# Optimization experiments

Measured on AMD Instinct MI355X. Metric: run time of the kernel, lower is better.

The kernel has to match this reference:

```python
import jax, jax.numpy as jnp
import numpy as np

SPARSITY = 0.8
NEG_INF = -1e10


def setup_inputs() -> dict:
    key = jax.random.key(0)
    k1, k2 = jax.random.split(key)
    B, N, C = 8, 2048, 768
    x = jax.random.normal(k1, (B, N, C), dtype=jnp.float32)
    # torch nn.Linear weight layout: [out_features, in_features] = [3C, C]
    Wqkv = jax.random.normal(k2, (3 * C, C), dtype=jnp.float32) * (1.0 / np.sqrt(C))
    return {"x": x, "Wqkv": Wqkv}


def reference(x, Wqkv):
    B, N, C = x.shape
    qkv = jnp.einsum('bnc,dc->bnd', x, Wqkv)  # [B, N, 3C]
    Q, K, V = jnp.split(qkv, 3, axis=-1)
    attn = jnp.einsum('bnc,bmc->bnm', Q, K) / jnp.sqrt(jnp.float32(C))  # [B,N,N]
    k = int(N * SPARSITY)
    _, idx = jax.lax.top_k(attn, k)  # [B, N, k]
    b_ix = jnp.arange(B)[:, None, None]
    n_ix = jnp.arange(N)[None, :, None]
    mask = jnp.zeros((B, N, N), dtype=bool).at[b_ix, n_ix, idx].set(True)
    attn = jnp.where(mask, attn, jnp.float32(NEG_INF))
    attn = jax.nn.softmax(attn, axis=-1)
    return jnp.einsum('bnm,bmc->bnc', attn, V)
```

## Files before the change

### kernel.cpp

```cpp
#include <hip/hip_runtime.h>
#include <hip/hip_bf16.h>
#include <math.h>


#define BM 128
#define BN 128
#define BK 64

typedef __attribute__((ext_vector_type(8))) short bf16x8;
typedef __attribute__((ext_vector_type(4))) float f32x4;

__device__ __forceinline__ unsigned short f2bf(float f) {
    unsigned u = __float_as_uint(f);
    unsigned r = u + 0x7FFFu + ((u >> 16) & 1u);
    return (unsigned short)(r >> 16);
}
__device__ __forceinline__ float bf2f(unsigned short h) {
    return __uint_as_float(((unsigned)h) << 16);
}

__device__ __forceinline__ void async16(const void* g, void* l) {
    __builtin_amdgcn_global_load_lds(
        (const __attribute__((address_space(1))) void*)g,
        (__attribute__((address_space(3))) void*)l, 16, 0, 0);
}

struct GemmArgs {
    const unsigned short* A0;
    const unsigned short* B0;
    int lda, ldb;
    long batchA, batchB;
    float alpha;
};

template <int EPI, int NT>
__global__ __launch_bounds__(256) void gemm_bf16(
    GemmArgs g, void* Cp0, void* Cp1, int ldc, long batchC)
{
    __shared__ unsigned short As[2][BM * BK];
    __shared__ unsigned short Bs[2][BN * BK];

    const int nx  = gridDim.x, ny = gridDim.y;
    const int nwg = nx * ny * gridDim.z;
    const int flat = blockIdx.x + nx * (blockIdx.y + ny * blockIdx.z);
    const int lid  = (flat & 7) * (nwg >> 3) + (flat >> 3);
    const int bx   = lid % nx;
    const int byz  = lid / nx;
    const int by   = byz % ny;
    const int bz   = byz / ny;

    const int t    = threadIdx.x;
    const int wid  = t >> 6, lane = t & 63;
    const int wr   = wid >> 1, wc = wid & 1;
    const int fr   = lane & 15, fq = lane >> 4;
    const int m0   = by * BM, n0 = bx * BN;

    const unsigned short* Ab0 = g.A0 + (long)bz * g.batchA + (long)m0 * g.lda;
    const unsigned short* Bb0 = g.B0 + (long)bz * g.batchB + (long)n0 * g.ldb;

    const int srow = t >> 3;
    const int sgc  = ((t & 7) ^ (srow & 7)) * 8;
    const char* pa[4];
    const char* pb[4];
#pragma unroll
    for (int i = 0; i < 4; ++i) {
        pa[i] = (const char*)(Ab0 + (long)(i * 32 + srow) * g.lda + sgc);
        pb[i] = (const char*)(Bb0 + (long)(i * 32 + srow) * g.ldb + sgc);
    }

    int aoffs[4][2], boffs[4][2];
#pragma unroll
    for (int m = 0; m < 4; ++m) {
        const int ra = wr * 64 + m * 16 + fr;
        const int rb = wc * 64 + m * 16 + fr;
#pragma unroll
        for (int ks = 0; ks < 2; ++ks) {
            aoffs[m][ks] = ra * 128 + (((ks * 4 + fq) ^ (ra & 7)) * 16);
            boffs[m][ks] = rb * 128 + (((ks * 4 + fq) ^ (rb & 7)) * 16);
        }
    }
    const char* AsBase = (const char*)&As[0][0];
    const char* BsBase = (const char*)&Bs[0][0];

    f32x4 acc[4][4];
#pragma unroll
    for (int m = 0; m < 4; ++m)
#pragma unroll
        for (int n = 0; n < 4; ++n) acc[m][n] = (f32x4)0.f;

    const int ldsT = wid * 1024;

#define STAGE(kt, u)                                                          \
    {                                                                         \
        _Pragma("unroll")                                                     \
        for (int i = 0; i < 4; ++i) {                                         \
            async16(pa[i] + (kt) * 128,                                       \
                    (char*)&As[(u)][0] + i * 4096 + ldsT);                    \
            async16(pb[i] + (kt) * 128,                                       \
                    (char*)&Bs[(u)][0] + i * 4096 + ldsT);                    \
        }                                                                     \
    }

    STAGE(0, 0);

#pragma unroll
    for (int tt = 0; tt < NT; ++tt) {
        if (tt + 1 < NT) {
            STAGE(tt + 1, (tt + 1) & 1);
            asm volatile("s_waitcnt vmcnt(8)" ::: "memory");
        } else {
            asm volatile("s_waitcnt vmcnt(0)" ::: "memory");
        }
        __builtin_amdgcn_sched_barrier(0);
        __builtin_amdgcn_s_barrier();
        __builtin_amdgcn_sched_barrier(0);

        const int bufo = (tt & 1) * 16384;
        bf16x8 fA[4][2], fB[4][2];
#pragma unroll
        for (int m = 0; m < 4; ++m)
#pragma unroll
            for (int ks = 0; ks < 2; ++ks) {
                fA[m][ks] = *(const bf16x8*)(AsBase + bufo + aoffs[m][ks]);
                fB[m][ks] = *(const bf16x8*)(BsBase + bufo + boffs[m][ks]);
            }
        __builtin_amdgcn_s_setprio(1);
#pragma unroll
        for (int m = 0; m < 4; ++m)
#pragma unroll
            for (int n = 0; n < 4; ++n)
#pragma unroll
                for (int ks = 0; ks < 2; ++ks)
                    acc[m][n] = __builtin_amdgcn_mfma_f32_16x16x32_bf16(
                        fA[m][ks], fB[n][ks], acc[m][n], 0, 0, 0);
        __builtin_amdgcn_s_setprio(0);
        __builtin_amdgcn_sched_barrier(0);
        __builtin_amdgcn_s_barrier();
        __builtin_amdgcn_sched_barrier(0);
    }
#undef STAGE

#pragma unroll
    for (int m = 0; m < 4; ++m) {
        const int gr0 = m0 + wr * 64 + m * 16 + fq * 4;
#pragma unroll
        for (int n = 0; n < 4; ++n) {
            const int gc = n0 + wc * 64 + n * 16 + fr;
            if (EPI == 0) {
                float* Cf = (float*)Cp0 + (long)bz * batchC;
#pragma unroll
                for (int j = 0; j < 4; ++j)
                    Cf[(long)(gr0 + j) * ldc + gc] = g.alpha * acc[m][n][j];
            } else if (EPI == 4) {
                unsigned short* H = (unsigned short*)Cp0 + (long)bz * batchC;
#pragma unroll
                for (int j = 0; j < 4; ++j)
                    H[(long)(gr0 + j) * ldc + gc] = f2bf(g.alpha * acc[m][n][j]);
            } else {
                if (n0 < 1536) {
                    unsigned short* H = (unsigned short*)Cp0;
#pragma unroll
                    for (int j = 0; j < 4; ++j)
                        H[(long)(gr0 + j) * ldc + gc] = f2bf(acc[m][n][j]);
                } else {
                    unsigned short* Vt = (unsigned short*)Cp1;
                    ushort4 p;
                    p.x = f2bf(acc[m][n][0]); p.y = f2bf(acc[m][n][1]);
                    p.z = f2bf(acc[m][n][2]); p.w = f2bf(acc[m][n][3]);
                    const long idx =
                        ((long)(gr0 >> 11) * 768 + (gc - 1536)) * 2048 + (gr0 & 2047);
                    *(ushort4*)&Vt[idx] = p;
                }
            }
        }
    }
}

__global__ __launch_bounds__(256) void cast_bf16(
    const float* __restrict__ in, unsigned short* __restrict__ outp, int n8)
{
    const int i = blockIdx.x * 256 + threadIdx.x;
    if (i >= n8) return;
    const float4 a = ((const float4*)in)[i * 2];
    const float4 b = ((const float4*)in)[i * 2 + 1];
    ushort4 h0, h1;
    h0.x = f2bf(a.x); h0.y = f2bf(a.y); h0.z = f2bf(a.z); h0.w = f2bf(a.w);
    h1.x = f2bf(b.x); h1.y = f2bf(b.y); h1.z = f2bf(b.z); h1.w = f2bf(b.w);
    ((ushort4*)outp)[i * 2]     = h0;
    ((ushort4*)outp)[i * 2 + 1] = h1;
}

#define ROWN 2048

__global__ __launch_bounds__(256) void topk_softmax_rows(
    const unsigned short* __restrict__ Sb, unsigned short* __restrict__ P,
    int kkeep)
{
    __shared__ __align__(16) unsigned hist[2048];
    __shared__ float    redmax[4], redmin[4], ssum[4];
    __shared__ unsigned wsum[4];
    __shared__ unsigned selBin;

    const unsigned short* row = Sb + (long)blockIdx.x * ROWN;
    unsigned short* prow = P + (long)blockIdx.x * ROWN;
    const int t    = threadIdx.x;
    const int lane = t & 63, w = t >> 6;

    float x[8];
    {
        const ushort4 a = ((const ushort4*)row)[t * 2];
        const ushort4 b = ((const ushort4*)row)[t * 2 + 1];
        x[0] = bf2f(a.x); x[1] = bf2f(a.y); x[2] = bf2f(a.z); x[3] = bf2f(a.w);
        x[4] = bf2f(b.x); x[5] = bf2f(b.y); x[6] = bf2f(b.z); x[7] = bf2f(b.w);
    }
    ((uint4*)hist)[t * 2]     = make_uint4(0, 0, 0, 0);
    ((uint4*)hist)[t * 2 + 1] = make_uint4(0, 0, 0, 0);

    float mx = x[0], mn = x[0];
#pragma unroll
    for (int j = 1; j < 8; ++j) { mx = fmaxf(mx, x[j]); mn = fminf(mn, x[j]); }
#pragma unroll
    for (int off = 32; off >= 1; off >>= 1) {
        mx = fmaxf(mx, __shfl_xor(mx, off, 64));
        mn = fminf(mn, __shfl_xor(mn, off, 64));
    }
    if (lane == 0) { redmax[w] = mx; redmin[w] = mn; }
    __syncthreads();
    mx = fmaxf(fmaxf(redmax[0], redmax[1]), fmaxf(redmax[2], redmax[3]));
    mn = fminf(fminf(redmin[0], redmin[1]), fminf(redmin[2], redmin[3]));

    const float scale = 2047.0f / fmaxf(mx - mn, 1e-30f);
    int q[8];
#pragma unroll
    for (int j = 0; j < 8; ++j) {
        int v = (int)((x[j] - mn) * scale);
        q[j] = v < 0 ? 0 : (v > 2047 ? 2047 : v);
        atomicAdd(&hist[q[j]], 1u);
    }
    __syncthreads();

    const uint4 h0 = ((const uint4*)hist)[t * 2];
    const uint4 h1 = ((const uint4*)hist)[t * 2 + 1];
    const unsigned hv[8] = { h0.x, h0.y, h0.z, h0.w, h1.x, h1.y, h1.z, h1.w };
    unsigned loc = 0;
#pragma unroll
    for (int j = 0; j < 8; ++j) loc += hv[j];
    unsigned s = loc;
#pragma unroll
    for (int off = 1; off <= 32; off <<= 1) {
        const unsigned o = __shfl_down(s, off, 64);
        s += (lane + off < 64) ? o : 0u;
    }
    if (lane == 0) wsum[w] = s;
    const unsigned texcl = s - loc;
    __syncthreads();
    unsigned above = texcl;
#pragma unroll
    for (int w2 = 0; w2 < 4; ++w2)
        if (w2 > w) above += wsum[w2];
    {
        unsigned cum = above;
        int hit = -1;
#pragma unroll
        for (int j = 7; j >= 0; --j) {
            const unsigned sp = cum;
            cum += hv[j];
            if (cum >= (unsigned)kkeep && sp < (unsigned)kkeep) hit = 8 * t + j;
        }
        if (hit >= 0) selBin = (unsigned)hit;
    }
    __syncthreads();
    const int bstar = (int)selBin;

    float e[8];
    float sum = 0.f;
#pragma unroll
    for (int j = 0; j < 8; ++j) {
        e[j] = (q[j] >= bstar) ? __expf(x[j] - mx) : 0.f;
        sum += e[j];
    }
#pragma unroll
    for (int off = 32; off >= 1; off >>= 1)
        sum += __shfl_xor(sum, off, 64);
    if (lane == 0) ssum[w] = sum;
    __syncthreads();
    const float inv = 1.0f / (ssum[0] + ssum[1] + ssum[2] + ssum[3]);

    ushort4 o0, o1;
    o0.x = f2bf(e[0] * inv); o0.y = f2bf(e[1] * inv);
    o0.z = f2bf(e[2] * inv); o0.w = f2bf(e[3] * inv);
    o1.x = f2bf(e[4] * inv); o1.y = f2bf(e[5] * inv);
    o1.z = f2bf(e[6] * inv); o1.w = f2bf(e[7] * inv);
    ((ushort4*)prow)[t * 2]     = o0;
    ((ushort4*)prow)[t * 2 + 1] = o1;
}

extern "C" void kernel_launch(void* const* d_in, const int* in_sizes, int n_in,
                              void* d_out, int out_size, void* d_ws, size_t ws_size,
                              hipStream_t stream)
{
    const float* x = (const float*)d_in[0];
    const float* W = (const float*)d_in[1];
    float* out = (float*)d_out;

    const int B = 8, N = 2048, C = 768;
    const int M = B * N;
    const int kkeep = 1638;

    char* ws = (char*)d_ws;
    unsigned short* QKb = (unsigned short*)(ws);
    unsigned short* Vt  = (unsigned short*)(ws + 50331648);
    unsigned short* Sb  = (unsigned short*)(ws + 75497472);
    unsigned short* Pb  = (unsigned short*)(ws + 142606336);
    unsigned short* xb  = (unsigned short*)(ws + 75497472);
    unsigned short* Wb  = (unsigned short*)(ws + 100663296);

    cast_bf16<<<dim3(M * C / 8 / 256), 256, 0, stream>>>(x, xb, M * C / 8);
    cast_bf16<<<dim3(3 * C * C / 8 / 256), 256, 0, stream>>>(W, Wb, 3 * C * C / 8);

    {
        GemmArgs pa{};
        pa.A0 = xb; pa.B0 = Wb;
        pa.lda = C; pa.ldb = C; pa.batchA = 0; pa.batchB = 0;
        pa.alpha = 1.f;
        gemm_bf16<5, 12><<<dim3(2304 / BN, M / BM, 1), 256, 0, stream>>>(
            pa, QKb, Vt, 1536, 0);
    }
    {
        GemmArgs qk{};
        qk.A0 = QKb; qk.B0 = QKb + C;
        qk.lda = 1536; qk.ldb = 1536;
        qk.batchA = (long)N * 1536; qk.batchB = (long)N * 1536;
        qk.alpha = 1.0f / sqrtf((float)C);
        gemm_bf16<4, 12><<<dim3(N / BN, N / BM, 8), 256, 0, stream>>>(
            qk, Sb, nullptr, N, (long)N * N);
    }
    topk_softmax_rows<<<dim3(B * N), 256, 0, stream>>>(Sb, Pb, kkeep);

    {
        GemmArgs pv{};
        pv.A0 = Pb; pv.B0 = Vt;
        pv.lda = N; pv.ldb = N;
        pv.batchA = (long)N * N; pv.batchB = (long)C * N;
        pv.alpha = 1.f;
        gemm_bf16<0, 32><<<dim3(C / BN, N / BM, 8), 256, 0, stream>>>(
            pv, out, nullptr, C, (long)N * C);
    }
}
```

Baseline: 243.7 us.

## Add dedicated 256x256-tile 8-wave QK^T GEMM kernel with ping-pong LDS pipeline

Replaces the generic 128x128 GEMM for the Q·K^T score computation with a specialized 512-thread kernel using 256x256 tiles, double-buffered swizzled LDS, and interleaved async global-to-LDS loads with MFMA phases. It also remaps workgroup IDs across XCDs for better L2 locality. The larger tile increases operand reuse and arithmetic intensity but uses much more LDS (128KB) and registers, limiting occupancy to one workgroup per CU.

Measured after the change: 239.4 us. No clear change (-1.8%).

```diff
diff --git a/kernel.cpp b/kernel.cpp
--- a/kernel.cpp
+++ b/kernel.cpp
@@ -151,11 +151,6 @@
 #pragma unroll
                 for (int j = 0; j < 4; ++j)
                     Cf[(long)(gr0 + j) * ldc + gc] = g.alpha * acc[m][n][j];
-            } else if (EPI == 4) {
-                unsigned short* H = (unsigned short*)Cp0 + (long)bz * batchC;
-#pragma unroll
-                for (int j = 0; j < 4; ++j)
-                    H[(long)(gr0 + j) * ldc + gc] = f2bf(g.alpha * acc[m][n][j]);
             } else {
                 if (n0 < 1536) {
                     unsigned short* H = (unsigned short*)Cp0;
@@ -176,6 +171,164 @@
     }
 }
 
+template <int NITER>
+__global__ __launch_bounds__(512) void gemm_qk8(
+    const unsigned short* __restrict__ Aq, const unsigned short* __restrict__ Bk,
+    unsigned short* __restrict__ Sb, float alpha)
+{
+    __shared__ unsigned short As[2][256 * 64];
+    __shared__ unsigned short Bs[2][256 * 64];
+
+    const int nx  = gridDim.x, ny = gridDim.y;
+    const int nwg = nx * ny * gridDim.z;
+    const int flat = blockIdx.x + nx * (blockIdx.y + ny * blockIdx.z);
+    const int lid  = (flat & 7) * (nwg >> 3) + (flat >> 3);
+    const int bx   = lid % nx;
+    const int byz  = lid / nx;
+    const int by   = byz % ny;
+    const int bz   = byz / ny;
+
+    const int t    = threadIdx.x;
+    const int wid  = t >> 6, lane = t & 63;
+    const int wr   = wid >> 2, wc = wid & 3;
+    const int fr   = lane & 15, fq = lane >> 4;
+    const int m0   = by * 256, n0 = bx * 256;
+
+    const unsigned short* Ab0 = Aq + (long)bz * 2048 * 1536 + (long)m0 * 1536;
+    const unsigned short* Bb0 = Bk + (long)bz * 2048 * 1536 + (long)n0 * 1536;
+
+    const int srow = t >> 3;
+    const int sgc  = ((t & 7) ^ (srow & 7)) * 8;
+    const char* pa[4];
+    const char* pb[4];
+#pragma unroll
+    for (int i = 0; i < 4; ++i) {
+        pa[i] = (const char*)(Ab0 + (long)(i * 64 + srow) * 1536 + sgc);
+        pb[i] = (const char*)(Bb0 + (long)(i * 64 + srow) * 1536 + sgc);
+    }
+
+    const int xo0 = ((fq    ) ^ (fr & 7)) * 16;
+    const int xo1 = ((fq + 4) ^ (fr & 7)) * 16;
+    const int abase = (wr * 128 + fr) * 128;
+    const int bbase = (wc * 64  + fr) * 128;
+    const char* AsB = (const char*)&As[0][0];
+    const char* BsB = (const char*)&Bs[0][0];
+    const int ldsT = wid * 1024;
+
+    f32x4 acc[8][4];
+#pragma unroll
+    for (int m = 0; m < 8; ++m)
+#pragma unroll
+        for (int n = 0; n < 4; ++n) acc[m][n] = (f32x4)0.f;
+
+#define SA_(h, kt)                                                            \
+    { char* d = (char*)&As[(kt) & 1][0] + (h) * 16384 + ldsT;                 \
+      async16(pa[2 * (h)]     + (long)(kt) * 128, d);                         \
+      async16(pa[2 * (h) + 1] + (long)(kt) * 128, d + 8192); }
+#define SB_(h, kt)                                                            \
+    { char* d = (char*)&Bs[(kt) & 1][0] + (h) * 16384 + ldsT;                 \
+      async16(pb[2 * (h)]     + (long)(kt) * 128, d);                         \
+      async16(pb[2 * (h) + 1] + (long)(kt) * 128, d + 8192); }
+#define BARRIER { __builtin_amdgcn_sched_barrier(0);                          \
+                  __builtin_amdgcn_s_barrier();                               \
+                  __builtin_amdgcn_sched_barrier(0); }
+#define LG0 { asm volatile("s_waitcnt lgkmcnt(0)" ::: "memory");              \
+              __builtin_amdgcn_sched_barrier(0); }
+#define VM6 { asm volatile("s_waitcnt vmcnt(6)" ::: "memory");                \
+              __builtin_amdgcn_sched_barrier(0); }
+#define VM0 { asm volatile("s_waitcnt vmcnt(0)" ::: "memory");                \
+              __builtin_amdgcn_sched_barrier(0); }
+#define LDA4_(bp, mq)                                                         \
+    _Pragma("unroll") for (int mi = 0; mi < 4; ++mi) {                        \
+        fA[mi][0] = *(const bf16x8*)((bp) + abase + ((mq)*4+mi)*2048 + xo0);  \
+        fA[mi][1] = *(const bf16x8*)((bp) + abase + ((mq)*4+mi)*2048 + xo1);  \
+    }
+#define LDB2_(bp, nb)                                                         \
+    _Pragma("unroll") for (int ni = 0; ni < 2; ++ni) {                        \
+        fB[(nb)+ni][0] = *(const bf16x8*)((bp) + bbase + ((nb)+ni)*2048 + xo0);\
+        fB[(nb)+ni][1] = *(const bf16x8*)((bp) + bbase + ((nb)+ni)*2048 + xo1);\
+    }
+#define MM16_(mq, nq)                                                         \
+    __builtin_amdgcn_s_setprio(1);                                            \
+    _Pragma("unroll") for (int mi = 0; mi < 4; ++mi)                          \
+    _Pragma("unroll") for (int ni = 0; ni < 2; ++ni)                          \
+    _Pragma("unroll") for (int ks = 0; ks < 2; ++ks)                          \
+        acc[(mq)*4+mi][(nq)*2+ni] = __builtin_amdgcn_mfma_f32_16x16x32_bf16(  \
+            fA[mi][ks], fB[(nq)*2+ni][ks], acc[(mq)*4+mi][(nq)*2+ni], 0,0,0); \
+    __builtin_amdgcn_s_setprio(0);
+
+    SB_(0, 0); SB_(1, 0); SA_(0, 0); SA_(1, 0);
+    SB_(0, 1); SB_(1, 1); SA_(0, 1);
+    VM6; BARRIER;
+
+    bf16x8 fA[4][2], fB[4][2];
+#pragma unroll
+    for (int it = 0; it < NITER; ++it) {
+        const int tb = 2 * it + 1;
+        const bool last = (it == NITER - 1);
+        const char* A0p = AsB;
+        const char* B0p = BsB;
+        const char* A1p = AsB + 32768;
+        const char* B1p = BsB + 32768;
+
+        LDA4_(A0p, 0); LDB2_(B0p, 0);
+        SA_(1, tb);
+        BARRIER; LG0; MM16_(0, 0); BARRIER;
+
+        LDB2_(B0p, 2);
+        BARRIER; LG0; MM16_(0, 1); BARRIER;
+
+        LDA4_(A0p, 1);
+        if (!last) SB_(0, tb + 1);
+        BARRIER; LG0; MM16_(1, 0); BARRIER;
+
+        if (!last) { SB_(1, tb + 1); SA_(0, tb + 1); }
+        BARRIER;
+        MM16_(1, 1);
+        if (last) VM0 else VM6;
+        BARRIER;
+
+        LDA4_(A1p, 0); LDB2_(B1p, 0);
+        if (!last) SA_(1, tb + 1);
+        BARRIER; LG0; MM16_(0, 0); BARRIER;
+
+        LDB2_(B1p, 2);
+        BARRIER; LG0; MM16_(0, 1); BARRIER;
+
+        LDA4_(A1p, 1);
+        if (!last) SB_(0, tb + 2);
+        BARRIER; LG0; MM16_(1, 0); BARRIER;
+
+        if (!last) { SB_(1, tb + 2); SA_(0, tb + 2); }
+        BARRIER;
+        MM16_(1, 1);
+        if (last) VM0 else VM6;
+        BARRIER;
+    }
+#undef SA_
+#undef SB_
+#undef BARRIER
+#undef LG0
+#undef VM6
+#undef VM0
+#undef LDA4_
+#undef LDB2_
+#undef MM16_
+
+    unsigned short* H = Sb + (long)bz * 2048 * 2048;
+#pragma unroll
+    for (int m = 0; m < 8; ++m) {
+        const int gr0 = m0 + wr * 128 + m * 16 + fq * 4;
+#pragma unroll
+        for (int n = 0; n < 4; ++n) {
+            const int gc = n0 + wc * 64 + n * 16 + fr;
+#pragma unroll
+            for (int j = 0; j < 4; ++j)
+                H[(long)(gr0 + j) * 2048 + gc] = f2bf(alpha * acc[m][n][j]);
+        }
+    }
+}
+
 __global__ __launch_bounds__(256) void cast_bf16(
     const float* __restrict__ in, unsigned short* __restrict__ outp, int n8)
 {
@@ -312,8 +465,8 @@
     unsigned short* Vt  = (unsigned short*)(ws + 50331648);
     unsigned short* Sb  = (unsigned short*)(ws + 75497472);
     unsigned short* Pb  = (unsigned short*)(ws + 142606336);
-    unsigned short* xb  = (unsigned short*)(ws + 75497472);
-    unsigned short* Wb  = (unsigned short*)(ws + 100663296);
+    unsigned short* xb = (unsigned short*)(ws + 75497472);
+    unsigned short* Wb = (unsigned short*)(ws + 100663296);
 
     cast_bf16<<<dim3(M * C / 8 / 256), 256, 0, stream>>>(x, xb, M * C / 8);
     cast_bf16<<<dim3(3 * C * C / 8 / 256), 256, 0, stream>>>(W, Wb, 3 * C * C / 8);
@@ -326,15 +479,9 @@
         gemm_bf16<5, 12><<<dim3(2304 / BN, M / BM, 1), 256, 0, stream>>>(
             pa, QKb, Vt, 1536, 0);
     }
-    {
-        GemmArgs qk{};
-        qk.A0 = QKb; qk.B0 = QKb + C;
-        qk.lda = 1536; qk.ldb = 1536;
-        qk.batchA = (long)N * 1536; qk.batchB = (long)N * 1536;
-        qk.alpha = 1.0f / sqrtf((float)C);
-        gemm_bf16<4, 12><<<dim3(N / BN, N / BM, 8), 256, 0, stream>>>(
-            qk, Sb, nullptr, N, (long)N * N);
-    }
+    gemm_qk8<6><<<dim3(8, 8, 8), 512, 0, stream>>>(
+        QKb, QKb + C, Sb, 1.0f / sqrtf((float)C));
+
     topk_softmax_rows<<<dim3(B * N), 256, 0, stream>>>(Sb, Pb, kkeep);
 
     {
```
